# Performance work log

Measured on AMD Instinct MI355X. Metric: run time of the kernel, lower is better.

## Reference

```python
import jax, jax.numpy as jnp
import numpy as np

NEG_INF = -1000000000.0

def setup_inputs() -> dict:
    key = jax.random.key(0)
    k1, k2, k3, k4 = jax.random.split(key, 4)
    N, F_in, F_out, H = 4096, 256, 64, 4
    x = jax.random.normal(k1, (N, F_in), dtype=jnp.float32)
    adj = jax.random.randint(k2, (N, N), 0, 2, dtype=jnp.int32)
    W = jax.random.normal(k3, (H, F_in, F_out), dtype=jnp.float32) * 0.05
    a = jax.random.normal(k4, (H, 2 * F_out, 1), dtype=jnp.float32) * 0.05
    return {"x": x, "adj": adj, "W": W, "a": a}

def reference(x, adj, W, a):
    # x: [N, F_in], adj: [N, N] int, W: [H, F_in, F_out], a: [H, 2*F_out, 1]
    H, F_in, F_out = W.shape
    N = x.shape[0]
    h = jnp.einsum('nf,hfo->hno', x, W)              # [H, N, F_out]
    a1 = a[:, :F_out, 0]                             # [H, F_out] (dot with h_i part of concat)
    a2 = a[:, F_out:, 0]                             # [H, F_out] (dot with h_j part)
    f1 = jnp.einsum('hno,ho->hn', h, a1)             # [H, N]
    f2 = jnp.einsum('hno,ho->hn', h, a2)             # [H, N]
    e = f1[:, :, None] + f2[:, None, :]              # [H, N, N] == dot(concat(h_i,h_j), a)
    e = jnp.where(e >= 0, e, 0.2 * e)                # leaky_relu, slope 0.2
    mask = (adj == 0).astype(jnp.float32) * NEG_INF  # [N, N]
    alpha = jax.nn.softmax(e + mask[None], axis=-1)  # [H, N, N]
    # dropout deterministic (training=False) -> identity
    out = jnp.einsum('hij,hjo->hio', alpha, h)       # [H, N, F_out]
    # concat=True: concat heads along feature dim
    return jnp.transpose(out, (1, 0, 2)).reshape(N, H * F_out)
```

## Files before the change

kernel.cpp:

```cpp
#include <hip/hip_runtime.h>
#include <hip/hip_bf16.h>
#include <stdint.h>

#define LOG2E  1.4426950408889634f
#define LOG2E5 0.28853900817779268f

typedef __attribute__((ext_vector_type(4))) float f4;
typedef __attribute__((ext_vector_type(4))) int   i4;
typedef __attribute__((ext_vector_type(8))) short s8;
typedef __attribute__((ext_vector_type(4))) short s4;

#if defined(__has_builtin)
# if __has_builtin(__builtin_amdgcn_exp2f)
#  define EXP2F(x) __builtin_amdgcn_exp2f(x)
# else
#  define EXP2F(x) exp2f(x)
# endif
#else
# define EXP2F(x) exp2f(x)
#endif

static __device__ __forceinline__ uint32_t fbits(float f) {
  union { float f; uint32_t u; } c; c.f = f; return c.u;
}
static __device__ __forceinline__ float ubits(uint32_t u) {
  union { uint32_t u; float f; } c; c.u = u; return c.f;
}
static __device__ __forceinline__ uint16_t bf16_rne(float f) {
  uint32_t b = fbits(f);
  b += 0x7FFFu + ((b >> 16) & 1u);
  return (uint16_t)(b >> 16);
}
static __device__ __forceinline__ float bf2f(uint16_t u) {
  return ubits(((uint32_t)u) << 16);
}
static __device__ __forceinline__ uint32_t fkey(float f) {
  uint32_t u = fbits(f);
  return (u >> 31) ? ~u : (u | 0x80000000u);
}
static __device__ __forceinline__ float unkey(uint32_t k) {
  return ubits((k & 0x80000000u) ? (k ^ 0x80000000u) : ~k);
}

__global__ __launch_bounds__(256) void k_pack_prep(
    const int* __restrict__ adj, uint32_t* __restrict__ bitsR,
    const float* __restrict__ W, uint16_t* __restrict__ WT,
    uint32_t* __restrict__ f2mkey) {
  int b = blockIdx.x;
  if (b < 2048) {
    int id = b * 256 + threadIdx.x;
    const int* src = adj + ((size_t)id << 5);
    i4 v[8];
    #pragma unroll
    for (int m = 0; m < 8; ++m) v[m] = *(const i4*)(src + (m << 2));
    uint32_t w = 0;
    #pragma unroll
    for (int m = 0; m < 8; ++m) {
      w |= ((uint32_t)v[m].x) << (4 * m);
      w |= ((uint32_t)v[m].y) << (4 * m + 1);
      w |= ((uint32_t)v[m].z) << (4 * m + 2);
      w |= ((uint32_t)v[m].w) << (4 * m + 3);
    }
    bitsR[id] = w;
  } else {
    int bb = b - 2048;
    if (bb == 0 && threadIdx.x < 4) f2mkey[threadIdx.x] = 0u;
    int idx = (bb * 256 + threadIdx.x) * 4;
    f4 w = *(const f4*)(W + idx);
    int h = idx >> 14;
    int k = (idx >> 6) & 255;
    int o = idx & 63;
    uint16_t* base = WT + ((h << 6) + o) * 256 + k;
    base[0]   = bf16_rne(w.x);
    base[256] = bf16_rne(w.y);
    base[512] = bf16_rne(w.z);
    base[768] = bf16_rne(w.w);
  }
}

__global__ __launch_bounds__(256) void k_gemm_h(
    const float* __restrict__ x, const uint16_t* __restrict__ WT,
    const float* __restrict__ a,
    uint16_t* __restrict__ hTf, float* __restrict__ f1, float* __restrict__ f2,
    uint32_t* __restrict__ f2mkey) {
  const int N = 4096, K = 256;
  __shared__ uint16_t xs[16][264];
  int t = threadIdx.x;
  int i0 = blockIdx.x * 16;
  {
    int r = t >> 4, c = (t & 15) << 4;
    const float* src = x + (i0 + r) * K + c;
    union { uint16_t u[16]; s8 v[2]; } tmp;
    #pragma unroll
    for (int i = 0; i < 16; i += 4) {
      f4 v = *(const f4*)(src + i);
      tmp.u[i+0] = bf16_rne(v.x); tmp.u[i+1] = bf16_rne(v.y);
      tmp.u[i+2] = bf16_rne(v.z); tmp.u[i+3] = bf16_rne(v.w);
    }
    *(s8*)&xs[r][c]     = tmp.v[0];
    *(s8*)&xs[r][c + 8] = tmp.v[1];
  }
  __syncthreads();
  int wave = t >> 6, lane = t & 63, lr = lane & 15, lc = lane >> 4;
  f4 acc[4];
  #pragma unroll
  for (int cg = 0; cg < 4; ++cg) acc[cg] = (f4){0.f, 0.f, 0.f, 0.f};
  #pragma unroll
  for (int ks = 0; ks < 8; ++ks) {
    s8 af = *(const s8*)&xs[lr][ks * 32 + lc * 8];
    #pragma unroll
    for (int cg = 0; cg < 4; ++cg) {
      s8 bf = *(const s8*)(WT + ((wave << 6) + (cg << 4) + lr) * 256 + ks * 32 + lc * 8);
      acc[cg] = __builtin_amdgcn_mfma_f32_16x16x32_bf16(af, bf, acc[cg], 0, 0, 0);
    }
  }
  float p1[4] = {0, 0, 0, 0}, p2[4] = {0, 0, 0, 0};
  #pragma unroll
  for (int cg = 0; cg < 4; ++cg) {
    float a1v = a[wave * 128 + (cg << 4) + lr];
    float a2v = a[wave * 128 + 64 + (cg << 4) + lr];
    #pragma unroll
    for (int q = 0; q < 4; ++q) {
      p1[q] = fmaf(acc[cg][q], a1v, p1[q]);
      p2[q] = fmaf(acc[cg][q], a2v, p2[q]);
    }
  }
  #pragma unroll
  for (int m = 1; m <= 8; m <<= 1) {
    #pragma unroll
    for (int q = 0; q < 4; ++q) {
      p1[q] += __shfl_xor(p1[q], m, 64);
      p2[q] += __shfl_xor(p2[q], m, 64);
    }
  }
  if (lr == 0) {
    #pragma unroll
    for (int q = 0; q < 4; ++q) {
      f1[wave * N + i0 + (lc << 2) + q] = p1[q];
      f2[wave * N + i0 + (lc << 2) + q] = p2[q];
    }
  }
  float wm = fmaxf(fmaxf(p2[0], p2[1]), fmaxf(p2[2], p2[3]));
  wm = fmaxf(wm, __shfl_xor(wm, 16, 64));
  wm = fmaxf(wm, __shfl_xor(wm, 32, 64));
  if (lane == 0) atomicMax(&f2mkey[wave], fkey(wm));
  int b0 = (i0 & 31) + (lc << 2);
  int hi = b0 >> 3, e0 = b0 & 7;
  size_t cbase = ((size_t)(wave * 32 + (i0 >> 7)) * 4 + ((i0 >> 5) & 3)) << 2;
  #pragma unroll
  for (int cg = 0; cg < 4; ++cg) {
    union { uint16_t u[4]; s4 v; } h4;
    #pragma unroll
    for (int q = 0; q < 4; ++q) h4.u[q] = bf16_rne(acc[cg][q]);
    *(s4*)(hTf + ((cbase + cg) << 9) + ((hi << 4) + lr) * 8 + e0) = h4.v;
  }
}

__global__ __launch_bounds__(256, 4) void k_attn(
    const uint32_t* __restrict__ bitsR, const float* __restrict__ f1,
    const float* __restrict__ f2, const uint32_t* __restrict__ f2mkey,
    const uint16_t* __restrict__ hTf,
    uint16_t* __restrict__ Op, float* __restrict__ lp) {
  const int N = 4096;
  __shared__ uint32_t lb[128 * 20];
  int p  = blockIdx.x & 7;
  int hb = blockIdx.x >> 3;
  int h  = hb & 3;
  int rb = hb >> 2;
  int R0 = rb << 7;
  int t = threadIdx.x, wave = t >> 6, lane = t & 63, lr = lane & 15, lc = lane >> 4;
  int i0 = R0 + (wave << 5);
  int jbase = p << 9;
  int jw0 = p << 4;
  const int nch = 16;

  {
    int r = t >> 1, w8 = (t & 1) << 3;
    const uint32_t* src = bitsR + ((size_t)(R0 + r) << 7) + jw0 + w8;
    i4 v0 = *(const i4*)src;
    i4 v1 = *(const i4*)(src + 4);
    *(i4*)&lb[r * 20 + w8] = v0;
    *(i4*)&lb[r * 20 + w8 + 4] = v1;
  }

  float fm = unkey(f2mkey[h]);
  float d1[2], d2[2];
  #pragma unroll
  for (int g = 0; g < 2; ++g) {
    float f1v = f1[h * N + i0 + (g << 4) + lr];
    float s = f1v + fm;
    float M = fmaxf(s, 0.2f * s);
    d1[g] = fmaf(f1v, LOG2E, -M * LOG2E);
    d2[g] = fmaf(f1v, LOG2E5, -M * LOG2E);
  }
  f4 acc[2][4], accl[2];
  #pragma unroll
  for (int g = 0; g < 2; ++g) {
    accl[g] = (f4){0.f, 0.f, 0.f, 0.f};
    #pragma unroll
    for (int cg = 0; cg < 4; ++cg) acc[g][cg] = (f4){0.f, 0.f, 0.f, 0.f};
  }
  const s8 ones = {0x3F80, 0x3F80, 0x3F80, 0x3F80, 0x3F80, 0x3F80, 0x3F80, 0x3F80};

  const float* fb = f2 + h * N + jbase + (lc << 3);
  const uint16_t* hbase = hTf + ((size_t)(h * 512 + (jw0 << 2)) << 9) + lane * 8;
  const uint32_t* lbw = &lb[(wave << 5) * 20 + lr * 20];
  int sh = lc << 3;

  __syncthreads();

  f4 cf0 = *(const f4*)(fb), cf1 = *(const f4*)(fb + 4);
  s8 cb0 = *(const s8*)(hbase);
  s8 cb1 = *(const s8*)(hbase + 512);
  s8 cb2 = *(const s8*)(hbase + 1024);
  s8 cb3 = *(const s8*)(hbase + 1536);

  for (int c = 0; c < nch; ++c) {
    f4 nf0 = cf0, nf1 = cf1;
    s8 nb0 = cb0, nb1 = cb1, nb2 = cb2, nb3 = cb3;
    if (c + 1 < nch) {
      nf0 = *(const f4*)(fb + ((c + 1) << 5));
      nf1 = *(const f4*)(fb + ((c + 1) << 5) + 4);
      const uint16_t* hc = hbase + ((size_t)(c + 1) << 11);
      nb0 = *(const s8*)(hc);
      nb1 = *(const s8*)(hc + 512);
      nb2 = *(const s8*)(hc + 1024);
      nb3 = *(const s8*)(hc + 1536);
    }
    #pragma unroll
    for (int g = 0; g < 2; ++g) {
      uint32_t ws = lbw[g * 320 + c] >> sh;
      uint32_t eb[8];
      #pragma unroll
      for (int e = 0; e < 8; ++e) {
        float f2e = (e < 4) ? cf0[e] : cf1[e - 4];
        float arg = fmaxf(fmaf(f2e, LOG2E, d1[g]),
                          fmaf(f2e, LOG2E5, d2[g]));
        uint32_t msk = 0u - ((ws >> e) & 1u);
        eb[e] = (fbits(EXP2F(arg)) & msk) + 0x8000u;
      }
      union { uint32_t u[4]; s8 v; } af;
      #pragma unroll
      for (int i2 = 0; i2 < 4; ++i2)
        af.u[i2] = __builtin_amdgcn_perm(eb[2 * i2 + 1], eb[2 * i2], 0x07060302u);
      acc[g][0] = __builtin_amdgcn_mfma_f32_16x16x32_bf16(af.v, cb0, acc[g][0], 0, 0, 0);
      acc[g][1] = __builtin_amdgcn_mfma_f32_16x16x32_bf16(af.v, cb1, acc[g][1], 0, 0, 0);
      acc[g][2] = __builtin_amdgcn_mfma_f32_16x16x32_bf16(af.v, cb2, acc[g][2], 0, 0, 0);
      acc[g][3] = __builtin_amdgcn_mfma_f32_16x16x32_bf16(af.v, cb3, acc[g][3], 0, 0, 0);
      accl[g]   = __builtin_amdgcn_mfma_f32_16x16x32_bf16(af.v, ones, accl[g], 0, 0, 0);
    }
    cf0 = nf0; cf1 = nf1;
    cb0 = nb0; cb1 = nb1; cb2 = nb2; cb3 = nb3;
  }

  size_t orow = (size_t)(((p << 2) + h) << 6);
  #pragma unroll
  for (int g = 0; g < 2; ++g) {
    #pragma unroll
    for (int cg = 0; cg < 4; ++cg) {
      union { uint16_t u[4]; s4 v; } h4;
      #pragma unroll
      for (int q = 0; q < 4; ++q) h4.u[q] = bf16_rne(acc[g][cg][q]);
      *(s4*)(Op + ((orow + (cg << 4) + lr) << 12) + i0 + (g << 4) + (lc << 2)) = h4.v;
    }
    if (lr == 0)
      *(f4*)(lp + ((size_t)((p << 2) + h) << 12) + i0 + (g << 4) + (lc << 2)) = accl[g];
  }
}

__global__ __launch_bounds__(256) void k_combine(
    const uint16_t* __restrict__ Op, const float* __restrict__ lp,
    float* __restrict__ out) {
  const int NP = 8;
  __shared__ float lt[64][65];
  __shared__ float lsv[64];
  int h = blockIdx.x >> 6, it = blockIdx.x & 63;
  int t = threadIdx.x;
  int o16 = t >> 4, ic = (t & 15) << 2;
  f4 a0 = {0,0,0,0}, a1 = a0, a2 = a0, a3 = a0;
  for (int p = 0; p < NP; ++p) {
    const uint16_t* base = Op + (((size_t)(((p << 2) + h) << 6) + o16) << 12)
                              + (it << 6) + ic;
    s4 v0 = *(const s4*)(base);
    s4 v1 = *(const s4*)(base + ((size_t)16 << 12));
    s4 v2 = *(const s4*)(base + ((size_t)32 << 12));
    s4 v3 = *(const s4*)(base + ((size_t)48 << 12));
    #pragma unroll
    for (int e = 0; e < 4; ++e) {
      a0[e] += bf2f((uint16_t)v0[e]);
      a1[e] += bf2f((uint16_t)v1[e]);
      a2[e] += bf2f((uint16_t)v2[e]);
      a3[e] += bf2f((uint16_t)v3[e]);
    }
  }
  *(f4*)&lt[o16][ic]      = a0;
  *(f4*)&lt[16 + o16][ic] = a1;
  *(f4*)&lt[32 + o16][ic] = a2;
  *(f4*)&lt[48 + o16][ic] = a3;
  if (t < 64) {
    float s = 0.f;
    for (int p = 0; p < NP; ++p)
      s += lp[((size_t)((p << 2) + h) << 12) + (it << 6) + t];
    lsv[t] = (s > 0.f) ? 1.0f / s : 0.f;
  }
  __syncthreads();
  int i = t >> 2, og = (t & 3) << 4;
  float inv = lsv[i];
  float* dst = out + (size_t)((it << 6) + i) * 256 + (h << 6) + og;
  #pragma unroll
  for (int s = 0; s < 4; ++s) {
    f4 r;
    #pragma unroll
    for (int e = 0; e < 4; ++e) r[e] = lt[og + (s << 2) + e][i] * inv;
    *(f4*)(dst + (s << 2)) = r;
  }
}

extern "C" void kernel_launch(void* const* d_in, const int* in_sizes, int n_in,
                              void* d_out, int out_size, void* d_ws, size_t ws_size,
                              hipStream_t stream) {
  (void)in_sizes; (void)n_in; (void)out_size; (void)ws_size;
  const float* x   = (const float*)d_in[0];
  const int*   adj = (const int*)d_in[1];
  const float* W   = (const float*)d_in[2];
  const float* a   = (const float*)d_in[3];
  float* out = (float*)d_out;
  char* ws = (char*)d_ws;

  size_t oWT = 0;
  size_t oHT = oWT + 131072;
  size_t oF1 = oHT + 2097152;
  size_t oF2 = oF1 + 65536;
  size_t oFM = oF2 + 65536;
  size_t oBT = (oFM + 16 + 255) & ~(size_t)255;
  size_t oOP = oBT + 2097152;
  size_t oLP = oOP + 16777216;

  uint16_t* WT    = (uint16_t*)(ws + oWT);
  uint16_t* hTf   = (uint16_t*)(ws + oHT);
  float*    f1    = (float*)(ws + oF1);
  float*    f2    = (float*)(ws + oF2);
  uint32_t* f2mk  = (uint32_t*)(ws + oFM);
  uint32_t* bitsR = (uint32_t*)(ws + oBT);
  uint16_t* Op    = (uint16_t*)(ws + oOP);
  float*    lp    = (float*)(ws + oLP);

  k_pack_prep<<<2112, 256, 0, stream>>>(adj, bitsR, W, WT, f2mk);
  k_gemm_h<<<256, 256, 0, stream>>>(x, WT, a, hTf, f1, f2, f2mk);
  k_attn<<<1024, 256, 0, stream>>>(bitsR, f1, f2, f2mk, hTf, Op, lp);
  k_combine<<<256, 256, 0, stream>>>(Op, lp, out);
}
```

Baseline: 69.37 us.

## Fuse split-K combine into attention kernel via in-block LDS reduction

Each attention block now covers 16 rows of one head, and its 4 waves each take a quarter of the 4096 columns instead of splitting columns across 8 blocks. Partial outputs and row sums are reduced through shared memory, then normalized and written straight to the final output. This removes the 16 MB bf16 partial buffer, the partial-sum buffer and the separate combine kernel. In exchange each wave issues only one MFMA group per chunk, which lowers reuse of the loaded h tiles: every block streams the full hTf slice for its head, so global reads of h rise, and the output writes are scattered 4-byte stores.

```diff
diff --git a/kernel.cpp b/kernel.cpp
--- a/kernel.cpp
+++ b/kernel.cpp
@@ -30,9 +30,6 @@
   uint32_t b = fbits(f);
   b += 0x7FFFu + ((b >> 16) & 1u);
   return (uint16_t)(b >> 16);
-}
-static __device__ __forceinline__ float bf2f(uint16_t u) {
-  return ubits(((uint32_t)u) << 16);
 }
 static __device__ __forceinline__ uint32_t fkey(float f) {
   uint32_t u = fbits(f);
@@ -159,52 +156,38 @@
 __global__ __launch_bounds__(256, 4) void k_attn(
     const uint32_t* __restrict__ bitsR, const float* __restrict__ f1,
     const float* __restrict__ f2, const uint32_t* __restrict__ f2mkey,
-    const uint16_t* __restrict__ hTf,
-    uint16_t* __restrict__ Op, float* __restrict__ lp) {
+    const uint16_t* __restrict__ hTf, float* __restrict__ out) {
   const int N = 4096;
-  __shared__ uint32_t lb[128 * 20];
-  int p  = blockIdx.x & 7;
-  int hb = blockIdx.x >> 3;
-  int h  = hb & 3;
-  int rb = hb >> 2;
-  int R0 = rb << 7;
-  int t = threadIdx.x, wave = t >> 6, lane = t & 63, lr = lane & 15, lc = lane >> 4;
-  int i0 = R0 + (wave << 5);
-  int jbase = p << 9;
-  int jw0 = p << 4;
-  const int nch = 16;
+  __shared__ uint32_t lb[16][132];
+  __shared__ float Ored[4][64][18];
+  __shared__ float lred[4][16];
+  int h = blockIdx.x & 3, rb = blockIdx.x >> 2;
+  int R0 = rb << 4;
+  int t = threadIdx.x, wq = t >> 6, lane = t & 63, lr = lane & 15, lc = lane >> 4;
 
   {
-    int r = t >> 1, w8 = (t & 1) << 3;
-    const uint32_t* src = bitsR + ((size_t)(R0 + r) << 7) + jw0 + w8;
+    int r = t >> 4, w8 = (t & 15) << 3;
+    const uint32_t* src = bitsR + ((size_t)(R0 + r) << 7) + w8;
     i4 v0 = *(const i4*)src;
     i4 v1 = *(const i4*)(src + 4);
-    *(i4*)&lb[r * 20 + w8] = v0;
-    *(i4*)&lb[r * 20 + w8 + 4] = v1;
+    *(i4*)&lb[r][w8]     = v0;
+    *(i4*)&lb[r][w8 + 4] = v1;
   }
 
   float fm = unkey(f2mkey[h]);
-  float d1[2], d2[2];
-  #pragma unroll
-  for (int g = 0; g < 2; ++g) {
-    float f1v = f1[h * N + i0 + (g << 4) + lr];
-    float s = f1v + fm;
-    float M = fmaxf(s, 0.2f * s);
-    d1[g] = fmaf(f1v, LOG2E, -M * LOG2E);
-    d2[g] = fmaf(f1v, LOG2E5, -M * LOG2E);
-  }
-  f4 acc[2][4], accl[2];
-  #pragma unroll
-  for (int g = 0; g < 2; ++g) {
-    accl[g] = (f4){0.f, 0.f, 0.f, 0.f};
-    #pragma unroll
-    for (int cg = 0; cg < 4; ++cg) acc[g][cg] = (f4){0.f, 0.f, 0.f, 0.f};
-  }
+  float f1v = f1[h * N + R0 + lr];
+  float s = f1v + fm;
+  float M = fmaxf(s, 0.2f * s);
+  float d1 = fmaf(f1v, LOG2E, -M * LOG2E);
+  float d2 = fmaf(f1v, LOG2E5, -M * LOG2E);
+
+  f4 acc[4], accl = {0.f, 0.f, 0.f, 0.f};
+  #pragma unroll
+  for (int cg = 0; cg < 4; ++cg) acc[cg] = (f4){0.f, 0.f, 0.f, 0.f};
   const s8 ones = {0x3F80, 0x3F80, 0x3F80, 0x3F80, 0x3F80, 0x3F80, 0x3F80, 0x3F80};
 
-  const float* fb = f2 + h * N + jbase + (lc << 3);
-  const uint16_t* hbase = hTf + ((size_t)(h * 512 + (jw0 << 2)) << 9) + lane * 8;
-  const uint32_t* lbw = &lb[(wave << 5) * 20 + lr * 20];
+  const float* fb = f2 + h * N + (wq << 10) + (lc << 3);
+  const uint16_t* hbase = hTf + (((size_t)(h * 512) + (wq << 7)) << 9) + lane * 8;
   int sh = lc << 3;
 
   __syncthreads();
@@ -215,10 +198,10 @@
   s8 cb2 = *(const s8*)(hbase + 1024);
   s8 cb3 = *(const s8*)(hbase + 1536);
 
-  for (int c = 0; c < nch; ++c) {
+  for (int c = 0; c < 32; ++c) {
     f4 nf0 = cf0, nf1 = cf1;
     s8 nb0 = cb0, nb1 = cb1, nb2 = cb2, nb3 = cb3;
-    if (c + 1 < nch) {
+    if (c + 1 < 32) {
       nf0 = *(const f4*)(fb + ((c + 1) << 5));
       nf1 = *(const f4*)(fb + ((c + 1) << 5) + 4);
       const uint16_t* hc = hbase + ((size_t)(c + 1) << 11);
@@ -227,92 +210,47 @@
       nb2 = *(const s8*)(hc + 1024);
       nb3 = *(const s8*)(hc + 1536);
     }
-    #pragma unroll
-    for (int g = 0; g < 2; ++g) {
-      uint32_t ws = lbw[g * 320 + c] >> sh;
-      uint32_t eb[8];
-      #pragma unroll
-      for (int e = 0; e < 8; ++e) {
-        float f2e = (e < 4) ? cf0[e] : cf1[e - 4];
-        float arg = fmaxf(fmaf(f2e, LOG2E, d1[g]),
-                          fmaf(f2e, LOG2E5, d2[g]));
-        uint32_t msk = 0u - ((ws >> e) & 1u);
-        eb[e] = (fbits(EXP2F(arg)) & msk) + 0x8000u;
-      }
-      union { uint32_t u[4]; s8 v; } af;
-      #pragma unroll
-      for (int i2 = 0; i2 < 4; ++i2)
-        af.u[i2] = __builtin_amdgcn_perm(eb[2 * i2 + 1], eb[2 * i2], 0x07060302u);
-      acc[g][0] = __builtin_amdgcn_mfma_f32_16x16x32_bf16(af.v, cb0, acc[g][0], 0, 0, 0);
-      acc[g][1] = __builtin_amdgcn_mfma_f32_16x16x32_bf16(af.v, cb1, acc[g][1], 0, 0, 0);
-      acc[g][2] = __builtin_amdgcn_mfma_f32_16x16x32_bf16(af.v, cb2, acc[g][2], 0, 0, 0);
-      acc[g][3] = __builtin_amdgcn_mfma_f32_16x16x32_bf16(af.v, cb3, acc[g][3], 0, 0, 0);
-      accl[g]   = __builtin_amdgcn_mfma_f32_16x16x32_bf16(af.v, ones, accl[g], 0, 0, 0);
-    }
+    uint32_t ws = lb[lr][(wq << 5) + c] >> sh;
+    uint32_t eb[8];
+    #pragma unroll
+    for (int e = 0; e < 8; ++e) {
+      float f2e = (e < 4) ? cf0[e] : cf1[e - 4];
+      float arg = fmaxf(fmaf(f2e, LOG2E, d1),
+                        fmaf(f2e, LOG2E5, d2));
+      uint32_t msk = 0u - ((ws >> e) & 1u);
+      eb[e] = (fbits(EXP2F(arg)) & msk) + 0x8000u;
+    }
+    union { uint32_t u[4]; s8 v; } af;
+    #pragma unroll
+    for (int i2 = 0; i2 < 4; ++i2)
+      af.u[i2] = __builtin_amdgcn_perm(eb[2 * i2 + 1], eb[2 * i2], 0x07060302u);
+    acc[0] = __builtin_amdgcn_mfma_f32_16x16x32_bf16(af.v, cb0, acc[0], 0, 0, 0);
+    acc[1] = __builtin_amdgcn_mfma_f32_16x16x32_bf16(af.v, cb1, acc[1], 0, 0, 0);
+    acc[2] = __builtin_amdgcn_mfma_f32_16x16x32_bf16(af.v, cb2, acc[2], 0, 0, 0);
+    acc[3] = __builtin_amdgcn_mfma_f32_16x16x32_bf16(af.v, cb3, acc[3], 0, 0, 0);
+    accl   = __builtin_amdgcn_mfma_f32_16x16x32_bf16(af.v, ones, accl, 0, 0, 0);
     cf0 = nf0; cf1 = nf1;
     cb0 = nb0; cb1 = nb1; cb2 = nb2; cb3 = nb3;
   }
 
-  size_t orow = (size_t)(((p << 2) + h) << 6);
-  #pragma unroll
-  for (int g = 0; g < 2; ++g) {
-    #pragma unroll
-    for (int cg = 0; cg < 4; ++cg) {
-      union { uint16_t u[4]; s4 v; } h4;
-      #pragma unroll
-      for (int q = 0; q < 4; ++q) h4.u[q] = bf16_rne(acc[g][cg][q]);
-      *(s4*)(Op + ((orow + (cg << 4) + lr) << 12) + i0 + (g << 4) + (lc << 2)) = h4.v;
-    }
-    if (lr == 0)
-      *(f4*)(lp + ((size_t)((p << 2) + h) << 12) + i0 + (g << 4) + (lc << 2)) = accl[g];
-  }
-}
-
-__global__ __launch_bounds__(256) void k_combine(
-    const uint16_t* __restrict__ Op, const float* __restrict__ lp,
-    float* __restrict__ out) {
-  const int NP = 8;
-  __shared__ float lt[64][65];
-  __shared__ float lsv[64];
-  int h = blockIdx.x >> 6, it = blockIdx.x & 63;
-  int t = threadIdx.x;
-  int o16 = t >> 4, ic = (t & 15) << 2;
-  f4 a0 = {0,0,0,0}, a1 = a0, a2 = a0, a3 = a0;
-  for (int p = 0; p < NP; ++p) {
-    const uint16_t* base = Op + (((size_t)(((p << 2) + h) << 6) + o16) << 12)
-                              + (it << 6) + ic;
-    s4 v0 = *(const s4*)(base);
-    s4 v1 = *(const s4*)(base + ((size_t)16 << 12));
-    s4 v2 = *(const s4*)(base + ((size_t)32 << 12));
-    s4 v3 = *(const s4*)(base + ((size_t)48 << 12));
-    #pragma unroll
-    for (int e = 0; e < 4; ++e) {
-      a0[e] += bf2f((uint16_t)v0[e]);
-      a1[e] += bf2f((uint16_t)v1[e]);
-      a2[e] += bf2f((uint16_t)v2[e]);
-      a3[e] += bf2f((uint16_t)v3[e]);
-    }
-  }
-  *(f4*)&lt[o16][ic]      = a0;
-  *(f4*)&lt[16 + o16][ic] = a1;
-  *(f4*)&lt[32 + o16][ic] = a2;
-  *(f4*)&lt[48 + o16][ic] = a3;
-  if (t < 64) {
-    float s = 0.f;
-    for (int p = 0; p < NP; ++p)
-      s += lp[((size_t)((p << 2) + h) << 12) + (it << 6) + t];
-    lsv[t] = (s > 0.f) ? 1.0f / s : 0.f;
-  }
+  #pragma unroll
+  for (int cg = 0; cg < 4; ++cg)
+    *(f4*)&Ored[wq][(cg << 4) + lr][lc << 2] = acc[cg];
+  if (lr == 0) *(f4*)&lred[wq][lc << 2] = accl;
   __syncthreads();
-  int i = t >> 2, og = (t & 3) << 4;
-  float inv = lsv[i];
-  float* dst = out + (size_t)((it << 6) + i) * 256 + (h << 6) + og;
-  #pragma unroll
-  for (int s = 0; s < 4; ++s) {
-    f4 r;
-    #pragma unroll
-    for (int e = 0; e < 4; ++e) r[e] = lt[og + (s << 2) + e][i] * inv;
-    *(f4*)(dst + (s << 2)) = r;
+
+  int o = t >> 2, ig = (t & 3) << 2;
+  f4 sum = {0.f, 0.f, 0.f, 0.f}, lsf = {0.f, 0.f, 0.f, 0.f};
+  #pragma unroll
+  for (int w = 0; w < 4; ++w) {
+    sum += *(const f4*)&Ored[w][o][ig];
+    lsf += *(const f4*)&lred[w][ig];
+  }
+  #pragma unroll
+  for (int k = 0; k < 4; ++k) {
+    float l = lsf[k];
+    float r = sum[k] * ((l > 0.f) ? 1.0f / l : 0.f);
+    out[(size_t)(R0 + ig + k) * 256 + (h << 6) + o] = r;
   }
 }
 
@@ -333,8 +271,6 @@
   size_t oF2 = oF1 + 65536;
   size_t oFM = oF2 + 65536;
   size_t oBT = (oFM + 16 + 255) & ~(size_t)255;
-  size_t oOP = oBT + 2097152;
-  size_t oLP = oOP + 16777216;
 
   uint16_t* WT    = (uint16_t*)(ws + oWT);
   uint16_t* hTf   = (uint16_t*)(ws + oHT);
@@ -342,11 +278,8 @@
   float*    f2    = (float*)(ws + oF2);
   uint32_t* f2mk  = (uint32_t*)(ws + oFM);
   uint32_t* bitsR = (uint32_t*)(ws + oBT);
-  uint16_t* Op    = (uint16_t*)(ws + oOP);
-  float*    lp    = (float*)(ws + oLP);
 
   k_pack_prep<<<2112, 256, 0, stream>>>(adj, bitsR, W, WT, f2mk);
   k_gemm_h<<<256, 256, 0, stream>>>(x, WT, a, hTf, f1, f2, f2mk);
-  k_attn<<<1024, 256, 0, stream>>>(bitsR, f1, f2, f2mk, hTf, Op, lp);
-  k_combine<<<256, 256, 0, stream>>>(Op, lp, out);
-}
+  k_attn<<<1024, 256, 0, stream>>>(bitsR, f1, f2, f2mk, hTf, out);
+}
```

Result: faster. 63.08 us (-9.1%).
